# Optimization experiments

Measured on AMD Instinct MI355X. Metric: run time of the kernel, lower is better.

The kernel has to match this reference:

```python
import jax, jax.numpy as jnp
import numpy as np

EMBED = 512
HEADS = 8
QKV = 64
HEAD_DIM = QKV // HEADS  # 8


def setup_inputs() -> dict:
    key = jax.random.key(0)
    ks = jax.random.split(key, 10)
    B, S = 8, 2048
    s = 1.0 / np.sqrt(EMBED)
    inp = {
        "x": jax.random.normal(ks[0], (B, S, EMBED), dtype=jnp.float32),
        "mask_matrix": jnp.zeros((S, S), dtype=jnp.float32),
        "Wq": jax.random.uniform(ks[1], (EMBED, QKV), jnp.float32, -s, s),
        "bq": jax.random.uniform(ks[2], (QKV,), jnp.float32, -s, s),
        "Wk": jax.random.uniform(ks[3], (EMBED, QKV), jnp.float32, -s, s),
        "bk": jax.random.uniform(ks[4], (QKV,), jnp.float32, -s, s),
        "Wv": jax.random.uniform(ks[5], (EMBED, QKV), jnp.float32, -s, s),
        "bv": jax.random.uniform(ks[6], (QKV,), jnp.float32, -s, s),
        "Wu": jax.random.uniform(ks[7], (QKV, EMBED), jnp.float32, -1.0 / 8.0, 1.0 / 8.0),
        "bu": jax.random.uniform(ks[8], (EMBED,), jnp.float32, -1.0 / 8.0, 1.0 / 8.0),
    }
    return inp


def reference(x, mask_matrix, Wq, bq, Wk, bk, Wv, bv, Wu, bu):
    B, S, _ = x.shape
    # projections to fixed 64-dim
    Q = x @ Wq + bq  # [B,S,64]
    K = x @ Wk + bk
    V = x @ Wv + bv
    # faithful reshape (NO head transpose, matching the original view chain)
    Q = Q.reshape(B * HEADS, S, HEAD_DIM)
    K = K.reshape(B * HEADS, S, HEAD_DIM)
    V = V.reshape(B * HEADS, S, HEAD_DIM)
    scores = jnp.einsum('gqd,gkd->gqk', Q, K)  # [B*H,S,S]
    scores = (scores + mask_matrix[None, :, :]) / np.sqrt(HEAD_DIM)
    probs = jax.nn.softmax(scores, axis=2)
    attn = jnp.einsum('gqk,gkd->gqd', probs, V)  # [B*H,S,hd]
    attn = attn.reshape(B, S, HEADS * HEAD_DIM)
    return attn @ Wu + bu
```

## Files before the change

### kernel.cpp

```cpp
#include <hip/hip_runtime.h>

typedef float f32x4 __attribute__((ext_vector_type(4)));
typedef float f32x16 __attribute__((ext_vector_type(16)));
typedef short s16x8 __attribute__((ext_vector_type(8)));
typedef unsigned int u32x2 __attribute__((ext_vector_type(2)));
typedef unsigned int u32x4 __attribute__((ext_vector_type(4)));

#define DEVFN static __device__ __forceinline__

constexpr int S_ = 2048;
constexpr int E_ = 512;
constexpr int D_ = 8;
constexpr int P_ = 64;
constexpr float C2 = 0.35355339059327373f * 1.4426950408889634f;


constexpr size_t FLAGA_OFF = 0;
constexpr size_t ZERO_OFF  = 1024;
constexpr size_t WT_OFF    = 2048;
constexpr size_t WUT_OFF   = WT_OFF + (size_t)192 * 512 * 2;
constexpr size_t QG_OFF    = WUT_OFF + (size_t)512 * 64 * 2;
constexpr size_t KG_OFF    = QG_OFF + (size_t)64 * 2048 * 8 * 2;
constexpr size_t VTG_OFF   = KG_OFF + (size_t)64 * 2048 * 8 * 2;

DEVFN short f2bf(float f) {
  unsigned u = __builtin_bit_cast(unsigned, f);
  return (short)((u + 0x7FFFu + ((u >> 16) & 1u)) >> 16);
}

DEVFN unsigned pkbf(float lo, float hi) {
  unsigned r;
  asm("v_cvt_pk_bf16_f32 %0, %1, %2" : "=v"(r) : "v"(lo), "v"(hi));
  return r;
}

DEVFN float fexp2(float x) {
#if __has_builtin(__builtin_amdgcn_exp2f)
  return __builtin_amdgcn_exp2f(x);
#else
  return exp2f(x);
#endif
}

DEVFN f32x16 mfma32(s16x8 a, s16x8 b, f32x16 c) {
  return __builtin_amdgcn_mfma_f32_32x32x16_bf16(a, b, c, 0, 0, 0);
}

DEVFN f32x16 zero16() {
  f32x16 z = {0,0,0,0,0,0,0,0,0,0,0,0,0,0,0,0};
  return z;
}

__global__ __launch_bounds__(256)
void prep_kernel(const float* __restrict__ Wq, const float* __restrict__ Wk,
                 const float* __restrict__ Wv, const float* __restrict__ Wu,
                 const float* __restrict__ maskm, short* __restrict__ WT,
                 short* __restrict__ WUT, int* __restrict__ flagA,
                 int* __restrict__ zerog)
{
  int bid = blockIdx.x, tid = threadIdx.x;
  if (bid == 0 && tid < 8) zerog[tid] = 0;
  if (bid < 48) {
    int base = (bid * 256 + tid) * 8;
#pragma unroll
    for (int j = 0; j < 8; ++j) {
      int idx = base + j;
      int n = idx >> 9, k = idx & 511;
      const float* W = (n < 64) ? Wq : ((n < 128) ? Wk : Wv);
      WT[idx] = f2bf(W[k * 64 + (n & 63)]);
    }
  } else if (bid < 56) {
    int base = ((bid - 48) * 256 + tid) * 16;
#pragma unroll
    for (int j = 0; j < 16; ++j) {
      int idx = base + j;
      int n = idx >> 6, k = idx & 63;
      WUT[idx] = f2bf(Wu[k * 512 + n]);
    }
  } else {
    __shared__ int bf_;
    if (tid == 0) bf_ = 0;
    __syncthreads();
    const f32x4* m4 = (const f32x4*)maskm;
    int base = (bid - 56) * 4096;
    unsigned any = 0;
#pragma unroll
    for (int i = 0; i < 16; ++i) {
      f32x4 v = m4[base + i * 256 + tid];
      any |= __builtin_bit_cast(unsigned, v[0]) | __builtin_bit_cast(unsigned, v[1])
           | __builtin_bit_cast(unsigned, v[2]) | __builtin_bit_cast(unsigned, v[3]);
    }
    if (any != 0) atomicOr(&bf_, 1);
    __syncthreads();
    if (tid == 0) flagA[bid - 56] = bf_;
  }
}

__global__ __launch_bounds__(384)
void proj_kernel(const float* __restrict__ x, const short* __restrict__ WT,
                 const float* __restrict__ bq, const float* __restrict__ bk,
                 const float* __restrict__ bv, short* __restrict__ QG,
                 short* __restrict__ KG, short* __restrict__ VTG)
{
  __shared__ short xl[32 * 520];
  int tid = threadIdx.x;
  int mb = blockIdx.x * 32;
  for (int i = tid; i < 32 * 128; i += 384) {
    int row = i >> 7, c4 = i & 127;
    f32x4 v = *(const f32x4*)(x + (size_t)(mb + row) * E_ + c4 * 4);
    u32x2 w;
    w[0] = pkbf(v[0], v[1]);
    w[1] = pkbf(v[2], v[3]);
    *(u32x2*)(&xl[row * 520 + c4 * 4]) = w;
  }
  __syncthreads();
  int lane = tid & 63, wvi = tid >> 6;
  int l31 = lane & 31, h = lane >> 5;
  int nstrip = wvi * 32;
  f32x16 acc = zero16();
#pragma unroll 4
  for (int kk = 0; kk < E_; kk += 16) {
    s16x8 af = *(const s16x8*)(WT + (size_t)(nstrip + l31) * E_ + kk + 8 * h);
    s16x8 bf = *(const s16x8*)(&xl[l31 * 520 + kk + 8 * h]);
    acc = mfma32(af, bf, acc);
  }
  int token = mb + l31;
  int bidx = token >> 11, s = token & 2047;
  int gg = bidx * 8 + (s >> 8);
#pragma unroll
  for (int i = 0; i < 4; ++i) {
    int n0 = nstrip + 8 * i + 4 * h;
    int proj = n0 >> 6;
    int wi = n0 & 63;
    int head = wi >> 3, db = wi & 7;
    const float* bias = (proj == 0) ? bq : ((proj == 1) ? bk : bv);
    float sc = (proj == 0) ? C2 : 1.0f;
    float f0 = (acc[4*i+0] + bias[wi+0]) * sc;
    float f1 = (acc[4*i+1] + bias[wi+1]) * sc;
    float f2 = (acc[4*i+2] + bias[wi+2]) * sc;
    float f3 = (acc[4*i+3] + bias[wi+3]) * sc;
    int p = ((s & 255) << 3) + head;
    if (proj == 2) {
      int k16 = p & 15;
      int slot = (k16 & 3) + ((k16 >> 2) & 1) * 8 + (k16 >> 3) * 4;
      size_t vb = (size_t)gg * (S_ * D_) + (size_t)(p >> 4) * 128 + slot;
      VTG[vb + (db+0)*16] = f2bf(f0);
      VTG[vb + (db+1)*16] = f2bf(f1);
      VTG[vb + (db+2)*16] = f2bf(f2);
      VTG[vb + (db+3)*16] = f2bf(f3);
    } else {
      short* dst = (proj == 0) ? QG : KG;
      u32x2 o;
      o[0] = pkbf(f0, f1);
      o[1] = pkbf(f2, f3);
      *(u32x2*)(dst + ((size_t)gg * S_ + p) * D_ + db) = o;
    }
  }
}

#define PAIR_BODY(kb, PREFETCH, USEMASK)                                \
  {                                                                     \
    f32x16 st0 = mfma32(kf0, qf, zero16());                             \
    f32x16 st1 = mfma32(kf1, qf, zero16());                             \
    s16x8 va0a = *(const s16x8*)vp0;                                    \
    s16x8 va0b = *(const s16x8*)vp1;                                    \
    s16x8 va1a = *(const s16x8*)vp2;                                    \
    s16x8 va1b = *(const s16x8*)vp3;                                    \
    vp0 += vstep; vp1 += vstep; vp2 += vstep; vp3 += vstep;             \
    if (PREFETCH) {                                                     \
      kf0 = *(const s16x8*)kptr;                                        \
      kf1 = *(const s16x8*)(kptr + kstride);                            \
      kptr += 2 * kstride;                                              \
    }                                                                   \
    float p0[16], p1[16];                                               \
    _Pragma("unroll")                                                   \
    for (int r = 0; r < 16; ++r) {                                      \
      float s0 = st0[r], s1 = st1[r];                                   \
      if (USEMASK) {                                                    \
        int key = (kb) + (r & 3) + 8 * (r >> 2) + 4 * h;                \
        s0 += maskm[(size_t)q * S_ + key] * C2;                         \
        s1 += maskm[(size_t)q * S_ + key + 32] * C2;                    \
      }                                                                 \
      p0[r] = fexp2(s0);                                                \
      p1[r] = fexp2(s1);                                                \
    }                                                                   \
    u32x4 b00, b01, b10, b11;                                           \
    b00[0] = pkbf(p0[0],  p0[1]);  b00[1] = pkbf(p0[2],  p0[3]);        \
    b00[2] = pkbf(p0[4],  p0[5]);  b00[3] = pkbf(p0[6],  p0[7]);        \
    b01[0] = pkbf(p0[8],  p0[9]);  b01[1] = pkbf(p0[10], p0[11]);       \
    b01[2] = pkbf(p0[12], p0[13]); b01[3] = pkbf(p0[14], p0[15]);       \
    b10[0] = pkbf(p1[0],  p1[1]);  b10[1] = pkbf(p1[2],  p1[3]);        \
    b10[2] = pkbf(p1[4],  p1[5]);  b10[3] = pkbf(p1[6],  p1[7]);        \
    b11[0] = pkbf(p1[8],  p1[9]);  b11[1] = pkbf(p1[10], p1[11]);       \
    b11[2] = pkbf(p1[12], p1[13]); b11[3] = pkbf(p1[14], p1[15]);       \
    __builtin_amdgcn_s_setprio(1);                                      \
    acc = mfma32(va0a, __builtin_bit_cast(s16x8, b00), acc);            \
    acc = mfma32(va0b, __builtin_bit_cast(s16x8, b01), acc);            \
    acc = mfma32(va1a, __builtin_bit_cast(s16x8, b10), acc);            \
    acc = mfma32(va1b, __builtin_bit_cast(s16x8, b11), acc);            \
    __builtin_amdgcn_s_setprio(0);                                      \
  }

__global__ __launch_bounds__(512, 4)
void attn_kernel(const short* __restrict__ QG, const short* __restrict__ KG,
                 const short* __restrict__ VTG, const float* __restrict__ maskm,
                 const int* __restrict__ flagA, const short* __restrict__ WUT,
                 const float* __restrict__ bu, float* __restrict__ out,
                 const short* __restrict__ zerog)
{
  __shared__ short V_lds[128 * 128];
  __shared__ float SP_lds[4][64][5];
  __shared__ short ones16[16];
  __shared__ int   sm_flag;
  short* A_lds = (short*)SP_lds;
  int bid = blockIdx.x;
  int xcd = bid & 7, idx = bid >> 3;
  int g  = xcd * 8 + (idx >> 4);
  int qb = (idx & 15) * 128;
  int tid = threadIdx.x;
  {
    const u32x4* vs = (const u32x4*)(VTG + (size_t)g * (S_ * D_));
    u32x4* vd = (u32x4*)V_lds;
#pragma unroll
    for (int it = 0; it < 4; ++it) {
      int i = tid + it * 512;
      vd[i] = vs[i];
    }
    if (tid < 8) ((unsigned*)ones16)[tid] = 0x3F803F80u;
    if (tid < 64) {
      const u32x4* fa4 = (const u32x4*)flagA;
      u32x4 f = fa4[tid];
      unsigned anyf = f[0] | f[1] | f[2] | f[3];
      unsigned long long bb = __ballot(anyf != 0);
      if (tid == 0) sm_flag = (bb != 0ull) ? 1 : 0;
    }
  }
  __syncthreads();

  int lane = tid & 63, wvi = tid >> 6;
  int l31 = lane & 31, h = lane >> 5;
  int strip = wvi & 3;
  int koff = (wvi >> 2) * 1024;
  int q = qb + strip * 32 + l31;
  bool hi = (h != 0);
  s16x8 zero8 = {0,0,0,0,0,0,0,0};

  s16x8 qf = hi ? zero8
                : *(const s16x8*)(QG + ((size_t)g * S_ + q) * D_);
  const short* kptr = hi ? zerog : (KG + ((size_t)g * S_ + koff + l31) * D_);
  int kstride = hi ? 0 : 32 * 8;
  bool realv = (l31 < 8);
  const short* vbase = realv ? &V_lds[(koff >> 4) * 128 + l31 * 16 + 8 * h]
                             : &ones16[8 * h];
  int voff  = realv ? 128 : 0;
  int vstep = 4 * voff;
  const short* vp0 = vbase;
  const short* vp1 = vbase + voff;
  const short* vp2 = vbase + 2 * voff;
  const short* vp3 = vbase + 3 * voff;
  f32x16 acc = zero16();
  bool usemask = (sm_flag != 0);

  s16x8 kf0 = *(const s16x8*)kptr;
  s16x8 kf1 = *(const s16x8*)(kptr + kstride);
  kptr += 2 * kstride;

  if (!usemask) {
    for (int kb = 0; kb < 1024 - 64; kb += 64) PAIR_BODY(koff + kb, true, false)
    PAIR_BODY(koff + 1024 - 64, false, false)
  } else {
    for (int kb = 0; kb < 1024 - 64; kb += 64) PAIR_BODY(koff + kb, true, true)
    PAIR_BODY(koff + 1024 - 64, false, true)
  }

  if (wvi >= 4) {
    SP_lds[strip][lane][0] = acc[0];
    SP_lds[strip][lane][1] = acc[1];
    SP_lds[strip][lane][2] = acc[2];
    SP_lds[strip][lane][3] = acc[3];
    SP_lds[strip][lane][4] = acc[4];
  }
  __syncthreads();
  float c0 = 0, c1 = 0, c2 = 0, c3 = 0, c4 = 0;
  if (wvi < 4) {
    c0 = SP_lds[strip][lane][0];
    c1 = SP_lds[strip][lane][1];
    c2 = SP_lds[strip][lane][2];
    c3 = SP_lds[strip][lane][3];
    c4 = SP_lds[strip][lane][4];
  }
  __syncthreads();
  if (wvi < 4) {
    float a0 = acc[0] + c0, a1 = acc[1] + c1;
    float a2 = acc[2] + c2, a3 = acc[3] + c3;
    float d0 = acc[4] + c4;
    float dp = __shfl_xor(d0, 32, 64);
    float den = hi ? dp : d0;
    float inv = __builtin_amdgcn_rcpf(den);
    u32x2 o;
    o[0] = pkbf(a0 * inv, a1 * inv);
    o[1] = pkbf(a2 * inv, a3 * inv);
    int local = strip * 4 + (l31 >> 3);
    int col = (l31 & 7) * 8 + 4 * h;
    *(u32x2*)(&A_lds[local * 68 + col]) = o;
  }
  __syncthreads();
  int nb = wvi * 64;
  f32x16 accA = zero16(), accB = zero16();
#pragma unroll
  for (int kk = 0; kk < 64; kk += 16) {
    s16x8 af  = *(const s16x8*)(&A_lds[l31 * 68 + kk + 8 * h]);
    s16x8 bfA = *(const s16x8*)(WUT + (size_t)(nb + l31) * P_ + kk + 8 * h);
    s16x8 bfB = *(const s16x8*)(WUT + (size_t)(nb + 32 + l31) * P_ + kk + 8 * h);
    accA = mfma32(af, bfA, accA);
    accB = mfma32(af, bfB, accB);
  }
  size_t token_base = (size_t)(g >> 3) * S_ + (g & 7) * 256 + (qb >> 3);
  size_t obase = token_base * E_;
  int nA = nb + l31, nB = nb + 32 + l31;
  float biasA = bu[nA], biasB = bu[nB];
#pragma unroll
  for (int r = 0; r < 8; ++r) {
    int m = (r & 3) + 8 * (r >> 2) + 4 * h;
    out[obase + (size_t)m * E_ + nA] = accA[r] + biasA;
    out[obase + (size_t)m * E_ + nB] = accB[r] + biasB;
  }
}

extern "C" void kernel_launch(void* const* d_in, const int* in_sizes, int n_in,
                              void* d_out, int out_size, void* d_ws, size_t ws_size,
                              hipStream_t stream) {
  const float* x     = (const float*)d_in[0];
  const float* maskm = (const float*)d_in[1];
  const float* Wq    = (const float*)d_in[2];
  const float* bq    = (const float*)d_in[3];
  const float* Wk    = (const float*)d_in[4];
  const float* bk    = (const float*)d_in[5];
  const float* Wv    = (const float*)d_in[6];
  const float* bv    = (const float*)d_in[7];
  const float* Wu    = (const float*)d_in[8];
  const float* bu    = (const float*)d_in[9];
  float* out = (float*)d_out;
  char* ws = (char*)d_ws;
  int*   flagA = (int*)(ws + FLAGA_OFF);
  int*   zerog = (int*)(ws + ZERO_OFF);
  short* WT    = (short*)(ws + WT_OFF);
  short* WUT   = (short*)(ws + WUT_OFF);
  short* QG    = (short*)(ws + QG_OFF);
  short* KG    = (short*)(ws + KG_OFF);
  short* VTG   = (short*)(ws + VTG_OFF);

  prep_kernel<<<312, 256, 0, stream>>>(Wq, Wk, Wv, Wu, maskm, WT, WUT, flagA, zerog);
  proj_kernel<<<512, 384, 0, stream>>>(x, WT, bq, bk, bv, QG, KG, VTG);
  attn_kernel<<<1024, 512, 0, stream>>>(QG, KG, VTG, maskm, flagA, WUT, bu, out,
                                        (const short*)zerog);
}
```

Measured before the change: 70.88 us.

## Double attention block size to 256 queries with 1024 threads per block

The attention kernel now uses 1024-thread blocks that each cover 256 queries of one group, halving the grid and the number of times each group's V tile is loaded into LDS. The combine step drops one barrier by reading partial sums straight from LDS, and the output projection is split across 16 waves with 32 columns each. The block-to-XCD swizzle changes to match. This amortizes V loads and block setup over more work, but fewer blocks may fit per CU and the larger blocks can hurt tail balance.

```diff
diff --git a/kernel.cpp b/kernel.cpp
--- a/kernel.cpp
+++ b/kernel.cpp
@@ -201,7 +201,7 @@
     __builtin_amdgcn_s_setprio(0);                                      \
   }
 
-__global__ __launch_bounds__(512, 4)
+__global__ __launch_bounds__(1024, 4)
 void attn_kernel(const short* __restrict__ QG, const short* __restrict__ KG,
                  const short* __restrict__ VTG, const float* __restrict__ maskm,
                  const int* __restrict__ flagA, const short* __restrict__ WUT,
@@ -209,21 +209,21 @@
                  const short* __restrict__ zerog)
 {
   __shared__ short V_lds[128 * 128];
-  __shared__ float SP_lds[4][64][5];
+  __shared__ float SP_lds[8][64][5];
+  __shared__ short A_lds[32 * 68];
   __shared__ short ones16[16];
   __shared__ int   sm_flag;
-  short* A_lds = (short*)SP_lds;
   int bid = blockIdx.x;
-  int xcd = bid & 7, idx = bid >> 3;
-  int g  = xcd * 8 + (idx >> 4);
-  int qb = (idx & 15) * 128;
+  int swz = (bid & 7) * 64 + (bid >> 3);
+  int g  = swz >> 3;
+  int qb = (swz & 7) * 256;
   int tid = threadIdx.x;
   {
     const u32x4* vs = (const u32x4*)(VTG + (size_t)g * (S_ * D_));
     u32x4* vd = (u32x4*)V_lds;
 #pragma unroll
-    for (int it = 0; it < 4; ++it) {
-      int i = tid + it * 512;
+    for (int it = 0; it < 2; ++it) {
+      int i = tid + it * 1024;
       vd[i] = vs[i];
     }
     if (tid < 8) ((unsigned*)ones16)[tid] = 0x3F803F80u;
@@ -239,8 +239,9 @@
 
   int lane = tid & 63, wvi = tid >> 6;
   int l31 = lane & 31, h = lane >> 5;
-  int strip = wvi & 3;
-  int koff = (wvi >> 2) * 1024;
+  int strip = wvi & 7;
+  int khalf = wvi >> 3;
+  int koff = khalf * 1024;
   int q = qb + strip * 32 + l31;
   bool hi = (h != 0);
   s16x8 zero8 = {0,0,0,0,0,0,0,0};
@@ -273,7 +274,7 @@
     PAIR_BODY(koff + 1024 - 64, false, true)
   }
 
-  if (wvi >= 4) {
+  if (khalf == 1) {
     SP_lds[strip][lane][0] = acc[0];
     SP_lds[strip][lane][1] = acc[1];
     SP_lds[strip][lane][2] = acc[2];
@@ -281,19 +282,12 @@
     SP_lds[strip][lane][4] = acc[4];
   }
   __syncthreads();
-  float c0 = 0, c1 = 0, c2 = 0, c3 = 0, c4 = 0;
-  if (wvi < 4) {
-    c0 = SP_lds[strip][lane][0];
-    c1 = SP_lds[strip][lane][1];
-    c2 = SP_lds[strip][lane][2];
-    c3 = SP_lds[strip][lane][3];
-    c4 = SP_lds[strip][lane][4];
-  }
-  __syncthreads();
-  if (wvi < 4) {
-    float a0 = acc[0] + c0, a1 = acc[1] + c1;
-    float a2 = acc[2] + c2, a3 = acc[3] + c3;
-    float d0 = acc[4] + c4;
+  if (khalf == 0) {
+    float a0 = acc[0] + SP_lds[strip][lane][0];
+    float a1 = acc[1] + SP_lds[strip][lane][1];
+    float a2 = acc[2] + SP_lds[strip][lane][2];
+    float a3 = acc[3] + SP_lds[strip][lane][3];
+    float d0 = acc[4] + SP_lds[strip][lane][4];
     float dp = __shfl_xor(d0, 32, 64);
     float den = hi ? dp : d0;
     float inv = __builtin_amdgcn_rcpf(den);
@@ -305,25 +299,22 @@
     *(u32x2*)(&A_lds[local * 68 + col]) = o;
   }
   __syncthreads();
-  int nb = wvi * 64;
-  f32x16 accA = zero16(), accB = zero16();
+  int nb = wvi * 32;
+  f32x16 accA = zero16();
 #pragma unroll
   for (int kk = 0; kk < 64; kk += 16) {
-    s16x8 af  = *(const s16x8*)(&A_lds[l31 * 68 + kk + 8 * h]);
-    s16x8 bfA = *(const s16x8*)(WUT + (size_t)(nb + l31) * P_ + kk + 8 * h);
-    s16x8 bfB = *(const s16x8*)(WUT + (size_t)(nb + 32 + l31) * P_ + kk + 8 * h);
-    accA = mfma32(af, bfA, accA);
-    accB = mfma32(af, bfB, accB);
+    s16x8 af = *(const s16x8*)(&A_lds[l31 * 68 + kk + 8 * h]);
+    s16x8 bf = *(const s16x8*)(WUT + (size_t)(nb + l31) * P_ + kk + 8 * h);
+    accA = mfma32(af, bf, accA);
   }
   size_t token_base = (size_t)(g >> 3) * S_ + (g & 7) * 256 + (qb >> 3);
   size_t obase = token_base * E_;
-  int nA = nb + l31, nB = nb + 32 + l31;
-  float biasA = bu[nA], biasB = bu[nB];
-#pragma unroll
-  for (int r = 0; r < 8; ++r) {
+  int nA = nb + l31;
+  float biasA = bu[nA];
+#pragma unroll
+  for (int r = 0; r < 16; ++r) {
     int m = (r & 3) + 8 * (r >> 2) + 4 * h;
     out[obase + (size_t)m * E_ + nA] = accA[r] + biasA;
-    out[obase + (size_t)m * E_ + nB] = accB[r] + biasB;
   }
 }
 
@@ -352,6 +343,6 @@
 
   prep_kernel<<<312, 256, 0, stream>>>(Wq, Wk, Wv, Wu, maskm, WT, WUT, flagA, zerog);
   proj_kernel<<<512, 384, 0, stream>>>(x, WT, bq, bk, bv, QG, KG, VTG);
-  attn_kernel<<<1024, 512, 0, stream>>>(QG, KG, VTG, maskm, flagA, WUT, bu, out,
+  attn_kernel<<<512, 1024, 0, stream>>>(QG, KG, VTG, maskm, flagA, WUT, bu, out,
                                         (const short*)zerog);
 }
```

New measurement: 69.57 us. Within noise of the previous version (-1.9%).
